# Optimization experiments

Hardware: AMD Instinct MI355X
Metric: run time of the kernel (lower is better)

Reference implementation:

```python
import jax, jax.numpy as jnp
import numpy as np

B_SZ, SEQ, H = 8, 1024, 2048
LN_EPS = 1e-6
CLIP = 1.0e6


def setup_inputs() -> dict:
    key = jax.random.key(0)
    ks = jax.random.split(key, 8)
    lecun = 1.0 / np.sqrt(H)
    return {
        "x": jax.random.normal(ks[0], (B_SZ, SEQ, H), dtype=jnp.float32),
        "context": jnp.zeros((B_SZ, H), dtype=jnp.float32),
        # learned params
        "A": -jax.random.uniform(ks[1], (H,), dtype=jnp.float32),  # diagonal decay (zeros-init in src; small negative for stable decay)
        "Bm": jax.random.normal(ks[2], (H, H), dtype=jnp.float32) * lecun,
        "Cm": jax.random.normal(ks[3], (H, H), dtype=jnp.float32) * lecun,
        "dt_kernel": jax.random.normal(ks[4], (H, 1), dtype=jnp.float32) * 0.02,
        "dt_bias": jnp.zeros((1,), dtype=jnp.float32),
        "gate_kernel": jax.random.normal(ks[5], (H, H), dtype=jnp.float32) * lecun,
        "gate_bias": jnp.zeros((H,), dtype=jnp.float32),
        "ln_scale": jnp.ones((H,), dtype=jnp.float32),
        "ln_bias": jnp.zeros((H,), dtype=jnp.float32),
    }


def _layernorm(x, scale, bias):
    mu = jnp.mean(x, axis=-1, keepdims=True)
    var = jnp.mean(jnp.square(x - mu), axis=-1, keepdims=True)
    return (x - mu) * jax.lax.rsqrt(var + LN_EPS) * scale + bias


def reference(x, context, A, Bm, Cm, dt_kernel, dt_bias, gate_kernel, gate_bias, ln_scale, ln_bias):
    xn = jnp.clip(_layernorm(x, ln_scale, ln_bias), -CLIP, CLIP)  # [B,S,H]
    xt = jnp.swapaxes(xn, 0, 1)  # time-major [S,B,H]

    def step(state, x_t):
        # x_t: [B,H]; delta: [B,1] from Dense(1)
        delta = jnp.exp(x_t @ dt_kernel + dt_bias)
        decay = jnp.exp(delta * A)                  # [B,H] via broadcast
        new_state = state * decay + x_t @ Bm        # [B,H]
        out = new_state @ Cm                        # [B,H]
        return new_state, out

    final_state, ys = jax.lax.scan(step, context, xt)
    outputs = jnp.swapaxes(ys, 0, 1)  # [B,S,H]
    gate = outputs @ gate_kernel + gate_bias
    outputs = outputs * jax.nn.sigmoid(gate)  # GLU
    # dropout deterministic (training=False) -> identity
    return outputs, final_state
```

## Files before the change

kernel.cpp:

```cpp
#include <hip/hip_runtime.h>
#include <hip/hip_bf16.h>

#define H_DIM 2048
#define B_SZ  8
#define SEQ   1024
#define M_DIM (B_SZ*SEQ)
#define KDIM  2048
#define NKT   (KDIM/64)
#define CCH   32
#define CLEN  (SEQ/CCH)

using f32x4 = __attribute__((ext_vector_type(4))) float;
using s16x8 = __attribute__((ext_vector_type(8))) short;

__device__ __forceinline__ float bf2f(unsigned short u) {
  unsigned int x = ((unsigned int)u) << 16;
  return __builtin_bit_cast(float, x);
}
__device__ __forceinline__ unsigned short f2bf(float f) {
  unsigned int x = __builtin_bit_cast(unsigned int, f);
  unsigned int r = (x + 0x7fffu + ((x >> 16) & 1u)) >> 16;
  return (unsigned short)r;
}

__device__ __forceinline__ void gl_lds16(const void* g, void* l) {
  __builtin_amdgcn_global_load_lds(
      (__attribute__((address_space(1))) void*)g,
      (__attribute__((address_space(3))) void*)l, 16, 0, 0);
}

__global__ __launch_bounds__(256) void transpose_kernel(
    const float* __restrict__ src, unsigned short* __restrict__ dst, int R, int C)
{
  __shared__ float t[32][33];
  int tx = threadIdx.x & 31, ty = threadIdx.x >> 5;
  int c0 = blockIdx.x << 5, r0 = blockIdx.y << 5;
#pragma unroll
  for (int i = 0; i < 32; i += 8)
    t[ty + i][tx] = src[(size_t)(r0 + ty + i) * C + (c0 + tx)];
  __syncthreads();
#pragma unroll
  for (int i = 0; i < 32; i += 8)
    dst[(size_t)(c0 + ty + i) * R + (r0 + tx)] = f2bf(t[tx][ty + i]);
}

__global__ __launch_bounds__(256) void ln_delta_kernel(
    const float* __restrict__ x, const float* __restrict__ lns,
    const float* __restrict__ lnb, const float* __restrict__ dtk,
    const float* __restrict__ dtb, unsigned short* __restrict__ xn,
    float* __restrict__ delta)
{
  const int row = blockIdx.x;
  const int tid = threadIdx.x;
  const float* xr = x + (size_t)row * H_DIM;
  float v[8];
  *(float4*)&v[0] = ((const float4*)xr)[tid * 2];
  *(float4*)&v[4] = ((const float4*)xr)[tid * 2 + 1];
  float s1 = 0.f, s2 = 0.f;
#pragma unroll
  for (int j = 0; j < 8; ++j) { s1 += v[j]; s2 += v[j] * v[j]; }
  __shared__ float red[8];
#pragma unroll
  for (int off = 32; off; off >>= 1) {
    s1 += __shfl_down(s1, off);
    s2 += __shfl_down(s2, off);
  }
  if ((tid & 63) == 0) { red[tid >> 6] = s1; red[4 + (tid >> 6)] = s2; }
  __syncthreads();
  float mean = (red[0] + red[1] + red[2] + red[3]) * (1.0f / H_DIM);
  float var  = (red[4] + red[5] + red[6] + red[7]) * (1.0f / H_DIM) - mean * mean;
  float rstd = rsqrtf(var + 1e-6f);

  float sc[8], bi[8], dk[8];
  *(float4*)&sc[0] = ((const float4*)lns)[tid * 2];
  *(float4*)&sc[4] = ((const float4*)lns)[tid * 2 + 1];
  *(float4*)&bi[0] = ((const float4*)lnb)[tid * 2];
  *(float4*)&bi[4] = ((const float4*)lnb)[tid * 2 + 1];
  *(float4*)&dk[0] = ((const float4*)dtk)[tid * 2];
  *(float4*)&dk[4] = ((const float4*)dtk)[tid * 2 + 1];

  float dot = 0.f;
  s16x8 o;
#pragma unroll
  for (int j = 0; j < 8; ++j) {
    float xv = (v[j] - mean) * rstd * sc[j] + bi[j];
    xv = fminf(fmaxf(xv, -1.0e6f), 1.0e6f);
    dot += xv * dk[j];
    o[j] = (short)f2bf(xv);
  }
  *(s16x8*)(xn + (size_t)row * H_DIM + tid * 8) = o;

  __syncthreads();
#pragma unroll
  for (int off = 32; off; off >>= 1) dot += __shfl_down(dot, off);
  if ((tid & 63) == 0) red[tid >> 6] = dot;
  __syncthreads();
  if (tid == 0)
    delta[row] = __expf(red[0] + red[1] + red[2] + red[3] + dtb[0]);
}

__global__ __launch_bounds__(256) void scan1_kernel(
    const unsigned short* __restrict__ U, const float* __restrict__ delta,
    const float* __restrict__ Adiag, float* __restrict__ Q, float* __restrict__ P)
{
  const int h = blockIdx.x * 1024 + threadIdx.x * 4;
  const int c = blockIdx.y, b = blockIdx.z;
  const float4 a = *(const float4*)(Adiag + h);
  const unsigned short* u = U + ((size_t)b * SEQ + c * CLEN) * H_DIM + h;
  const float* dl = delta + b * SEQ + c * CLEN;
  float4 st = {0.f, 0.f, 0.f, 0.f};
  float4 pr = {1.f, 1.f, 1.f, 1.f};
#pragma unroll 8
  for (int s = 0; s < CLEN; ++s) {
    const float d = dl[s];
    const ushort4 uv = *(const ushort4*)(u + (size_t)s * H_DIM);
    const float dx = __expf(d * a.x), dy = __expf(d * a.y);
    const float dz = __expf(d * a.z), dw = __expf(d * a.w);
    st.x = fmaf(st.x, dx, bf2f(uv.x)); st.y = fmaf(st.y, dy, bf2f(uv.y));
    st.z = fmaf(st.z, dz, bf2f(uv.z)); st.w = fmaf(st.w, dw, bf2f(uv.w));
    pr.x *= dx; pr.y *= dy; pr.z *= dz; pr.w *= dw;
  }
  const size_t idx = ((size_t)b * CCH + c) * H_DIM + h;
  *(float4*)(Q + idx) = st;
  *(float4*)(P + idx) = pr;
}

__global__ __launch_bounds__(256) void scan2_kernel(
    const float* __restrict__ Q, const float* __restrict__ P,
    const float* __restrict__ ctx, float* __restrict__ sIn,
    float* __restrict__ finalSt)
{
  const int h = blockIdx.x * 256 + threadIdx.x;
  const int b = blockIdx.y;
  float s = ctx[b * H_DIM + h];
#pragma unroll
  for (int c = 0; c < CCH; ++c) {
    const size_t idx = ((size_t)b * CCH + c) * H_DIM + h;
    sIn[idx] = s;
    s = fmaf(s, P[idx], Q[idx]);
  }
  finalSt[b * H_DIM + h] = s;
}

__global__ __launch_bounds__(256) void scan3_kernel(
    const unsigned short* __restrict__ U, const float* __restrict__ delta,
    const float* __restrict__ Adiag, const float* __restrict__ sIn,
    unsigned short* __restrict__ states)
{
  const int h = blockIdx.x * 1024 + threadIdx.x * 4;
  const int c = blockIdx.y, b = blockIdx.z;
  const float4 a = *(const float4*)(Adiag + h);
  const unsigned short* u = U + ((size_t)b * SEQ + c * CLEN) * H_DIM + h;
  unsigned short* so = states + ((size_t)b * SEQ + c * CLEN) * H_DIM + h;
  const float* dl = delta + b * SEQ + c * CLEN;
  float4 st = *(const float4*)(sIn + ((size_t)b * CCH + c) * H_DIM + h);
#pragma unroll 8
  for (int s = 0; s < CLEN; ++s) {
    const float d = dl[s];
    const ushort4 uv = *(const ushort4*)(u + (size_t)s * H_DIM);
    const float dx = __expf(d * a.x), dy = __expf(d * a.y);
    const float dz = __expf(d * a.z), dw = __expf(d * a.w);
    st.x = fmaf(st.x, dx, bf2f(uv.x)); st.y = fmaf(st.y, dy, bf2f(uv.y));
    st.z = fmaf(st.z, dz, bf2f(uv.z)); st.w = fmaf(st.w, dw, bf2f(uv.w));
    ushort4 ov = { f2bf(st.x), f2bf(st.y), f2bf(st.z), f2bf(st.w) };
    *(ushort4*)(so + (size_t)s * H_DIM) = ov;
  }
}


#define BARR()  __builtin_amdgcn_s_barrier();
#define VMC(N)  asm volatile("s_waitcnt vmcnt(" #N ")" ::: "memory");

#define RD_A(DST, PL, PHH, OFF) { _Pragma("unroll") for (int i_ = 0; i_ < 4; ++i_) { \
    DST[0][i_] = *(const s16x8*)((PL) + (OFF) + i_ * 4096); \
    DST[1][i_] = *(const s16x8*)((PHH) + (OFF) + i_ * 4096); } }
#define RD_B(DST, PL, PHH, OFF) { _Pragma("unroll") for (int j_ = 0; j_ < 2; ++j_) { \
    DST[0][j_] = *(const s16x8*)((PL) + (OFF) + j_ * 8192); \
    DST[1][j_] = *(const s16x8*)((PHH) + (OFF) + j_ * 8192); } }

#define QMM(IB, JB, AF, BF) { __builtin_amdgcn_s_setprio(1); \
  _Pragma("unroll") for (int i_ = 0; i_ < 4; ++i_) \
  _Pragma("unroll") for (int j_ = 0; j_ < 2; ++j_) { \
    acc[(IB)+i_][(JB)+j_] = __builtin_amdgcn_mfma_f32_16x16x32_bf16(AF[0][i_], BF[0][j_], acc[(IB)+i_][(JB)+j_], 0, 0, 0); \
    acc[(IB)+i_][(JB)+j_] = __builtin_amdgcn_mfma_f32_16x16x32_bf16(AF[1][i_], BF[1][j_], acc[(IB)+i_][(JB)+j_], 0, 0, 0); } \
  __builtin_amdgcn_s_setprio(0); }

#define STAGE_A(BUF, HH, TT) { const char* s_ = srcA + (HH) * 524288 + (TT) * 128; \
  char* d_ = ldsA + (BUF) * 32768 + (HH) * 16384 + tid16; \
  gl_lds16(s_, d_); gl_lds16(s_ + 262144, d_ + 8192); }
#define STAGE_B(BUF, HH, TT) { const char* s_ = srcB + (HH) * 524288 + (TT) * 128; \
  char* d_ = ldsB + (BUF) * 32768 + (HH) * 16384 + tid16; \
  gl_lds16(s_, d_); gl_lds16(s_ + 262144, d_ + 8192); }

template <int EPI>
__global__ __launch_bounds__(512, 2) void gemm8p(
    const char* __restrict__ Ab, const char* __restrict__ Bb,
    float* __restrict__ outF, unsigned short* __restrict__ outH,
    const unsigned short* __restrict__ Ybf, const float* __restrict__ gbias)
{
  extern __shared__ char lds[];
  char* ldsA = lds;
  char* ldsB = lds + 65536;

  const int tid  = threadIdx.x;
  const int lane = tid & 63, wid = tid >> 6;
  const int wr = wid >> 2, wc = wid & 3;
  const int fr = lane & 15, kq = lane >> 4;

  const int bid = blockIdx.x;
  const int xcd = bid & 7;
  const int li  = bid >> 3;
  const int bm  = (xcd >> 1) * 8 + (li & 7);
  const int bn  = (xcd & 1) * 4 + (li >> 3);

  const int grow = tid >> 3;
  const int gswz = ((tid & 7) ^ (grow & 7)) << 4;
  const char* srcA = Ab + ((size_t)(bm * 256 + grow)) * 4096 + gswz;
  const char* srcB = Bb + ((size_t)(bn * 256 + grow)) * 4096 + gswz;
  const int tid16 = tid << 4;

  const int sw0 = ((kq ^ (fr & 7)) << 4);
  const int sw1 = (((4 | kq) ^ (fr & 7)) << 4);
  const char* pa0b0 = ldsA + wr * 2048 + fr * 128 + sw0;
  const char* pa1b0 = ldsA + wr * 2048 + fr * 128 + sw1;
  const char* pa0b1 = pa0b0 + 32768;
  const char* pa1b1 = pa1b0 + 32768;
  const char* pb0b0 = ldsB + wc * 2048 + fr * 128 + sw0;
  const char* pb1b0 = ldsB + wc * 2048 + fr * 128 + sw1;
  const char* pb0b1 = pb0b0 + 32768;
  const char* pb1b1 = pb1b0 + 32768;

  f32x4 acc[8][4] = {};
  s16x8 a03[2][4], a47[2][4], b01a[2][2], b01b[2][2], b23[2][2];

  STAGE_A(0, 0, 0); STAGE_B(0, 0, 0); STAGE_B(0, 1, 0); STAGE_A(0, 1, 0);
  STAGE_A(1, 0, 1); STAGE_B(1, 0, 1); STAGE_B(1, 1, 1);
  VMC(6);
  BARR();
  RD_A(a03, pa0b0, pa1b0, 0);
  RD_B(b01a, pb0b0, pb1b0, 0);

  for (int t = 0; t < NKT / 2 - 1; ++t) {
    const int T0 = 2 * t;
    RD_B(b23, pb0b0, pb1b0, 16384);
    STAGE_A(1, 1, T0 + 1);
    QMM(0, 0, a03, b01a);
    VMC(6); BARR();
    RD_A(a47, pa0b0, pa1b0, 16384);
    STAGE_A(0, 0, T0 + 2);
    QMM(0, 2, a03, b23);
    VMC(6); BARR();
    RD_B(b01b, pb0b1, pb1b1, 0);
    STAGE_B(0, 0, T0 + 2);
    QMM(4, 0, a47, b01a);
    VMC(6); BARR();
    RD_A(a03, pa0b1, pa1b1, 0);
    STAGE_B(0, 1, T0 + 2);
    QMM(4, 2, a47, b23);
    VMC(6); BARR();
    RD_B(b23, pb0b1, pb1b1, 16384);
    STAGE_A(0, 1, T0 + 2);
    QMM(0, 0, a03, b01b);
    VMC(6); BARR();
    RD_A(a47, pa0b1, pa1b1, 16384);
    STAGE_A(1, 0, T0 + 3);
    QMM(0, 2, a03, b23);
    VMC(6); BARR();
    RD_B(b01a, pb0b0, pb1b0, 0);
    STAGE_B(1, 0, T0 + 3);
    QMM(4, 0, a47, b01b);
    VMC(6); BARR();
    RD_A(a03, pa0b0, pa1b0, 0);
    STAGE_B(1, 1, T0 + 3);
    QMM(4, 2, a47, b23);
    VMC(6); BARR();
  }

  RD_B(b23, pb0b0, pb1b0, 16384);
  STAGE_A(1, 1, 31);
  QMM(0, 0, a03, b01a);
  VMC(6); BARR();
  RD_A(a47, pa0b0, pa1b0, 16384);
  QMM(0, 2, a03, b23);
  VMC(0); BARR();
  RD_B(b01b, pb0b1, pb1b1, 0);
  QMM(4, 0, a47, b01a);
  RD_A(a03, pa0b1, pa1b1, 0);
  QMM(4, 2, a47, b23);
  RD_B(b23, pb0b1, pb1b1, 16384);
  QMM(0, 0, a03, b01b);
  RD_A(a47, pa0b1, pa1b1, 16384);
  QMM(0, 2, a03, b23);
  QMM(4, 0, a47, b01b);
  QMM(4, 2, a47, b23);

  __syncthreads();
  const int cr = (lane >> 4) << 2;
  const int cc = lane & 15;
  if constexpr (EPI == 1) {
#pragma unroll
    for (int i = 0; i < 8; ++i)
#pragma unroll
      for (int j = 0; j < 4; ++j)
#pragma unroll
        for (int r = 0; r < 4; ++r) {
          const int row = (2 * i + wr) * 16 + cr + r;
          const int col = (4 * j + wc) * 16 + cc;
          const int off = (row * 512 + col * 2) ^ ((row & 7) << 4);
          *(unsigned short*)(lds + off) = f2bf(acc[i][j][r]);
        }
    __syncthreads();
#pragma unroll
    for (int it = 0; it < 16; ++it) {
      const int L = it * 8192 + tid * 16;
      const int row = L >> 9, inrow = L & 511;
      const s16x8 v = *(const s16x8*)(lds + (L ^ ((row & 7) << 4)));
      *(s16x8*)(outH + ((size_t)(bm * 256 + row)) * H_DIM + bn * 256 + (inrow >> 1)) = v;
    }
  } else {
#pragma unroll
    for (int p = 0; p < 2; ++p) {
      if (p) __syncthreads();
#pragma unroll
      for (int i = 4 * p; i < 4 * p + 4; ++i)
#pragma unroll
        for (int j = 0; j < 4; ++j)
#pragma unroll
          for (int r = 0; r < 4; ++r) {
            const int lrow = (2 * i + wr) * 16 + cr + r - 128 * p;
            const int col = (4 * j + wc) * 16 + cc;
            const int off = (lrow * 1024 + col * 4) ^ ((lrow & 7) << 4);
            *(float*)(lds + off) = acc[i][j][r];
          }
      __syncthreads();
#pragma unroll
      for (int it = 0; it < 16; ++it) {
        const int L = it * 8192 + tid * 16;
        const int lrow = L >> 10, inrow = L & 1023;
        const f32x4 v = *(const f32x4*)(lds + (L ^ ((lrow & 7) << 4)));
        const size_t growg = (size_t)(bm * 256 + 128 * p + lrow);
        const int gcol = bn * 256 + (inrow >> 2);
        const float4 gb4 = *(const float4*)(gbias + gcol);
        const ushort4 y4 = *(const ushort4*)(Ybf + growg * H_DIM + gcol);
        float4 o;
        o.x = bf2f(y4.x) / (1.f + __expf(-(v[0] + gb4.x)));
        o.y = bf2f(y4.y) / (1.f + __expf(-(v[1] + gb4.y)));
        o.z = bf2f(y4.z) / (1.f + __expf(-(v[2] + gb4.z)));
        o.w = bf2f(y4.w) / (1.f + __expf(-(v[3] + gb4.w)));
        *(float4*)(outF + growg * H_DIM + gcol) = o;
      }
    }
  }
}

extern "C" void kernel_launch(void* const* d_in, const int* in_sizes, int n_in,
                              void* d_out, int out_size, void* d_ws, size_t ws_size,
                              hipStream_t stream) {
  (void)in_sizes; (void)n_in; (void)out_size; (void)ws_size;
  const float* x     = (const float*)d_in[0];
  const float* ctx   = (const float*)d_in[1];
  const float* Adiag = (const float*)d_in[2];
  const float* Bm    = (const float*)d_in[3];
  const float* Cm    = (const float*)d_in[4];
  const float* dtk   = (const float*)d_in[5];
  const float* dtb   = (const float*)d_in[6];
  const float* gk    = (const float*)d_in[7];
  const float* gb    = (const float*)d_in[8];
  const float* lns   = (const float*)d_in[9];
  const float* lnb   = (const float*)d_in[10];
  float* outF = (float*)d_out;

  char* ws = (char*)d_ws;
  unsigned short* xnY    = (unsigned short*)ws; ws += (size_t)M_DIM * H_DIM * 2;
  unsigned short* U      = (unsigned short*)ws; ws += (size_t)M_DIM * H_DIM * 2;
  unsigned short* states = (unsigned short*)ws; ws += (size_t)M_DIM * H_DIM * 2;
  unsigned short* T1     = (unsigned short*)ws; ws += (size_t)H_DIM * H_DIM * 2;
  unsigned short* T2     = (unsigned short*)ws; ws += (size_t)H_DIM * H_DIM * 2;
  unsigned short* T3     = (unsigned short*)ws; ws += (size_t)H_DIM * H_DIM * 2;
  float* delta           = (float*)ws;          ws += (size_t)M_DIM * 4;
  float* Qbuf            = (float*)ws;          ws += (size_t)B_SZ * CCH * H_DIM * 4;
  float* Pbuf            = (float*)ws;          ws += (size_t)B_SZ * CCH * H_DIM * 4;
  float* sInBuf          = (float*)ws;          ws += (size_t)B_SZ * CCH * H_DIM * 4;

  hipFuncSetAttribute((const void*)&gemm8p<1>,
                      hipFuncAttributeMaxDynamicSharedMemorySize, 131072);
  hipFuncSetAttribute((const void*)&gemm8p<2>,
                      hipFuncAttributeMaxDynamicSharedMemorySize, 131072);

  dim3 tb(256);
  transpose_kernel<<<dim3(64, 64), tb, 0, stream>>>(Bm, T1, H_DIM, H_DIM);
  transpose_kernel<<<dim3(64, 64), tb, 0, stream>>>(Cm, T2, H_DIM, H_DIM);
  transpose_kernel<<<dim3(64, 64), tb, 0, stream>>>(gk, T3, H_DIM, H_DIM);
  ln_delta_kernel<<<M_DIM, tb, 0, stream>>>(x, lns, lnb, dtk, dtb, xnY, delta);
  gemm8p<1><<<256, 512, 131072, stream>>>(
      (const char*)xnY, (const char*)T1, nullptr, U, nullptr, nullptr);
  scan1_kernel<<<dim3(H_DIM / 1024, CCH, B_SZ), tb, 0, stream>>>(
      U, delta, Adiag, Qbuf, Pbuf);
  scan2_kernel<<<dim3(H_DIM / 256, B_SZ), tb, 0, stream>>>(
      Qbuf, Pbuf, ctx, sInBuf, outF + (size_t)M_DIM * H_DIM);
  scan3_kernel<<<dim3(H_DIM / 1024, CCH, B_SZ), tb, 0, stream>>>(
      U, delta, Adiag, sInBuf, states);
  gemm8p<1><<<256, 512, 131072, stream>>>(
      (const char*)states, (const char*)T2, nullptr, xnY, nullptr, nullptr);
  gemm8p<2><<<256, 512, 131072, stream>>>(
      (const char*)xnY, (const char*)T3, outF, nullptr, xnY, gb);
}
```

Measured before the change: 259.7 us.

## Switch GEMM inner loop from 16x16x32 to 32x32x16 bf16 MFMA tiles

Rewrites the GEMM's fragment loads, MFMA calls and epilogue writeback to use 32x32x16 bf16 MFMA instructions instead of 16x16x32. Each wave now holds a 4x2 grid of 32x32 accumulators. Fragments are read per 32-row slab with a new swizzled K-offset table. Larger MFMA tiles cut the number of LDS fragment reads per FLOP and the instruction issue overhead. The risk is a different register footprint and possible LDS bank conflicts from the new access pattern.

```diff
diff --git a/kernel.cpp b/kernel.cpp
--- a/kernel.cpp
+++ b/kernel.cpp
@@ -10,8 +10,9 @@
 #define CCH   32
 #define CLEN  (SEQ/CCH)
 
-using f32x4 = __attribute__((ext_vector_type(4))) float;
-using s16x8 = __attribute__((ext_vector_type(8))) short;
+using f32x4  = __attribute__((ext_vector_type(4))) float;
+using f32x16 = __attribute__((ext_vector_type(16))) float;
+using s16x8  = __attribute__((ext_vector_type(8))) short;
 
 __device__ __forceinline__ float bf2f(unsigned short u) {
   unsigned int x = ((unsigned int)u) << 16;
@@ -171,18 +172,16 @@
 #define BARR()  __builtin_amdgcn_s_barrier();
 #define VMC(N)  asm volatile("s_waitcnt vmcnt(" #N ")" ::: "memory");
 
-#define RD_A(DST, PL, PHH, OFF) { _Pragma("unroll") for (int i_ = 0; i_ < 4; ++i_) { \
-    DST[0][i_] = *(const s16x8*)((PL) + (OFF) + i_ * 4096); \
-    DST[1][i_] = *(const s16x8*)((PHH) + (OFF) + i_ * 4096); } }
-#define RD_B(DST, PL, PHH, OFF) { _Pragma("unroll") for (int j_ = 0; j_ < 2; ++j_) { \
-    DST[0][j_] = *(const s16x8*)((PL) + (OFF) + j_ * 8192); \
-    DST[1][j_] = *(const s16x8*)((PHH) + (OFF) + j_ * 8192); } }
-
-#define QMM(IB, JB, AF, BF) { __builtin_amdgcn_s_setprio(1); \
-  _Pragma("unroll") for (int i_ = 0; i_ < 4; ++i_) \
-  _Pragma("unroll") for (int j_ = 0; j_ < 2; ++j_) { \
-    acc[(IB)+i_][(JB)+j_] = __builtin_amdgcn_mfma_f32_16x16x32_bf16(AF[0][i_], BF[0][j_], acc[(IB)+i_][(JB)+j_], 0, 0, 0); \
-    acc[(IB)+i_][(JB)+j_] = __builtin_amdgcn_mfma_f32_16x16x32_bf16(AF[1][i_], BF[1][j_], acc[(IB)+i_][(JB)+j_], 0, 0, 0); } \
+#define RD_AM(DST, BUF, MQ) { _Pragma("unroll") for (int m_ = 0; m_ < 2; ++m_) \
+  _Pragma("unroll") for (int s_ = 0; s_ < 4; ++s_) \
+    DST[m_][s_] = *(const s16x8*)(paA + (BUF) * 32768 + (MQ) * 16384 + m_ * 8192 + soff[s_]); }
+#define RD_BN(DST, BUF, N) { _Pragma("unroll") for (int s_ = 0; s_ < 4; ++s_) \
+    DST[s_] = *(const s16x8*)(pbB + (BUF) * 32768 + (N) * 16384 + soff[s_]); }
+
+#define QMM(AF, BF, MI, NI) { __builtin_amdgcn_s_setprio(1); \
+  _Pragma("unroll") for (int m_ = 0; m_ < 2; ++m_) \
+  _Pragma("unroll") for (int s_ = 0; s_ < 4; ++s_) \
+    acc[(MI)+m_][NI] = __builtin_amdgcn_mfma_f32_32x32x16_bf16(AF[m_][s_], BF[s_], acc[(MI)+m_][NI], 0, 0, 0); \
   __builtin_amdgcn_s_setprio(0); }
 
 #define STAGE_A(BUF, HH, TT) { const char* s_ = srcA + (HH) * 524288 + (TT) * 128; \
@@ -205,7 +204,7 @@
   const int tid  = threadIdx.x;
   const int lane = tid & 63, wid = tid >> 6;
   const int wr = wid >> 2, wc = wid & 3;
-  const int fr = lane & 15, kq = lane >> 4;
+  const int ln31 = lane & 31, l5 = lane >> 5;
 
   const int bid = blockIdx.x;
   const int xcd = bid & 7;
@@ -219,95 +218,90 @@
   const char* srcB = Bb + ((size_t)(bn * 256 + grow)) * 4096 + gswz;
   const int tid16 = tid << 4;
 
-  const int sw0 = ((kq ^ (fr & 7)) << 4);
-  const int sw1 = (((4 | kq) ^ (fr & 7)) << 4);
-  const char* pa0b0 = ldsA + wr * 2048 + fr * 128 + sw0;
-  const char* pa1b0 = ldsA + wr * 2048 + fr * 128 + sw1;
-  const char* pa0b1 = pa0b0 + 32768;
-  const char* pa1b1 = pa1b0 + 32768;
-  const char* pb0b0 = ldsB + wc * 2048 + fr * 128 + sw0;
-  const char* pb1b0 = ldsB + wc * 2048 + fr * 128 + sw1;
-  const char* pb0b1 = pb0b0 + 32768;
-  const char* pb1b1 = pb1b0 + 32768;
-
-  f32x4 acc[8][4] = {};
-  s16x8 a03[2][4], a47[2][4], b01a[2][2], b01b[2][2], b23[2][2];
+  const char* paA = ldsA + wr * 4096 + ln31 * 128;
+  const char* pbB = ldsB + (wc * 32 + ln31) * 128;
+  int soff[4];
+#pragma unroll
+  for (int s = 0; s < 4; ++s)
+    soff[s] = ((2 * s + l5) ^ (ln31 & 7)) << 4;
+
+  f32x16 acc[4][2] = {};
+  s16x8 aA[2][4], aB[2][4], bA[4], bB[4], bA2[4];
 
   STAGE_A(0, 0, 0); STAGE_B(0, 0, 0); STAGE_B(0, 1, 0); STAGE_A(0, 1, 0);
   STAGE_A(1, 0, 1); STAGE_B(1, 0, 1); STAGE_B(1, 1, 1);
   VMC(6);
   BARR();
-  RD_A(a03, pa0b0, pa1b0, 0);
-  RD_B(b01a, pb0b0, pb1b0, 0);
+  RD_AM(aA, 0, 0);
+  RD_BN(bA, 0, 0);
 
   for (int t = 0; t < NKT / 2 - 1; ++t) {
     const int T0 = 2 * t;
-    RD_B(b23, pb0b0, pb1b0, 16384);
+    RD_BN(bB, 0, 1);
     STAGE_A(1, 1, T0 + 1);
-    QMM(0, 0, a03, b01a);
-    VMC(6); BARR();
-    RD_A(a47, pa0b0, pa1b0, 16384);
+    QMM(aA, bA, 0, 0);
+    VMC(6); BARR();
+    RD_AM(aB, 0, 1);
     STAGE_A(0, 0, T0 + 2);
-    QMM(0, 2, a03, b23);
-    VMC(6); BARR();
-    RD_B(b01b, pb0b1, pb1b1, 0);
+    QMM(aA, bB, 0, 1);
+    VMC(6); BARR();
+    RD_BN(bA2, 1, 0);
     STAGE_B(0, 0, T0 + 2);
-    QMM(4, 0, a47, b01a);
-    VMC(6); BARR();
-    RD_A(a03, pa0b1, pa1b1, 0);
+    QMM(aB, bA, 2, 0);
+    VMC(6); BARR();
+    RD_AM(aA, 1, 0);
     STAGE_B(0, 1, T0 + 2);
-    QMM(4, 2, a47, b23);
-    VMC(6); BARR();
-    RD_B(b23, pb0b1, pb1b1, 16384);
+    QMM(aB, bB, 2, 1);
+    VMC(6); BARR();
+    RD_BN(bB, 1, 1);
     STAGE_A(0, 1, T0 + 2);
-    QMM(0, 0, a03, b01b);
-    VMC(6); BARR();
-    RD_A(a47, pa0b1, pa1b1, 16384);
+    QMM(aA, bA2, 0, 0);
+    VMC(6); BARR();
+    RD_AM(aB, 1, 1);
     STAGE_A(1, 0, T0 + 3);
-    QMM(0, 2, a03, b23);
-    VMC(6); BARR();
-    RD_B(b01a, pb0b0, pb1b0, 0);
+    QMM(aA, bB, 0, 1);
+    VMC(6); BARR();
+    RD_BN(bA, 0, 0);
     STAGE_B(1, 0, T0 + 3);
-    QMM(4, 0, a47, b01b);
-    VMC(6); BARR();
-    RD_A(a03, pa0b0, pa1b0, 0);
+    QMM(aB, bA2, 2, 0);
+    VMC(6); BARR();
+    RD_AM(aA, 0, 0);
     STAGE_B(1, 1, T0 + 3);
-    QMM(4, 2, a47, b23);
-    VMC(6); BARR();
-  }
-
-  RD_B(b23, pb0b0, pb1b0, 16384);
+    QMM(aB, bB, 2, 1);
+    VMC(6); BARR();
+  }
+
+  RD_BN(bB, 0, 1);
   STAGE_A(1, 1, 31);
-  QMM(0, 0, a03, b01a);
+  QMM(aA, bA, 0, 0);
   VMC(6); BARR();
-  RD_A(a47, pa0b0, pa1b0, 16384);
-  QMM(0, 2, a03, b23);
+  RD_AM(aB, 0, 1);
+  QMM(aA, bB, 0, 1);
   VMC(0); BARR();
-  RD_B(b01b, pb0b1, pb1b1, 0);
-  QMM(4, 0, a47, b01a);
-  RD_A(a03, pa0b1, pa1b1, 0);
-  QMM(4, 2, a47, b23);
-  RD_B(b23, pb0b1, pb1b1, 16384);
-  QMM(0, 0, a03, b01b);
-  RD_A(a47, pa0b1, pa1b1, 16384);
-  QMM(0, 2, a03, b23);
-  QMM(4, 0, a47, b01b);
-  QMM(4, 2, a47, b23);
+  RD_BN(bA2, 1, 0);
+  QMM(aB, bA, 2, 0);
+  RD_AM(aA, 1, 0);
+  QMM(aB, bB, 2, 1);
+  RD_BN(bB, 1, 1);
+  QMM(aA, bA2, 0, 0);
+  RD_AM(aB, 1, 1);
+  QMM(aA, bB, 0, 1);
+  QMM(aB, bA2, 2, 0);
+  QMM(aB, bB, 2, 1);
 
   __syncthreads();
-  const int cr = (lane >> 4) << 2;
-  const int cc = lane & 15;
   if constexpr (EPI == 1) {
 #pragma unroll
-    for (int i = 0; i < 8; ++i)
-#pragma unroll
-      for (int j = 0; j < 4; ++j)
-#pragma unroll
-        for (int r = 0; r < 4; ++r) {
-          const int row = (2 * i + wr) * 16 + cr + r;
-          const int col = (4 * j + wc) * 16 + cc;
+    for (int mi = 0; mi < 4; ++mi)
+#pragma unroll
+      for (int n = 0; n < 2; ++n)
+#pragma unroll
+        for (int reg = 0; reg < 16; ++reg) {
+          const int rowin = (reg & 3) + 8 * (reg >> 2) + 4 * l5;
+          const int row = (4 * (mi >> 1) + 2 * (mi & 1) + wr) * 32 + rowin;
+          const int col = n * 128 + wc * 32 + ln31;
           const int off = (row * 512 + col * 2) ^ ((row & 7) << 4);
-          *(unsigned short*)(lds + off) = f2bf(acc[i][j][r]);
+          *(unsigned short*)(lds + off) = f2bf(acc[mi][n][reg]);
         }
     __syncthreads();
 #pragma unroll
@@ -322,15 +316,16 @@
     for (int p = 0; p < 2; ++p) {
       if (p) __syncthreads();
 #pragma unroll
-      for (int i = 4 * p; i < 4 * p + 4; ++i)
-#pragma unroll
-        for (int j = 0; j < 4; ++j)
-#pragma unroll
-          for (int r = 0; r < 4; ++r) {
-            const int lrow = (2 * i + wr) * 16 + cr + r - 128 * p;
-            const int col = (4 * j + wc) * 16 + cc;
+      for (int mi = 2 * p; mi < 2 * p + 2; ++mi)
+#pragma unroll
+        for (int n = 0; n < 2; ++n)
+#pragma unroll
+          for (int reg = 0; reg < 16; ++reg) {
+            const int rowin = (reg & 3) + 8 * (reg >> 2) + 4 * l5;
+            const int lrow = (2 * (mi & 1) + wr) * 32 + rowin;
+            const int col = n * 128 + wc * 32 + ln31;
             const int off = (lrow * 1024 + col * 4) ^ ((lrow & 7) << 4);
-            *(float*)(lds + off) = acc[i][j][r];
+            *(float*)(lds + off) = acc[mi][n][reg];
           }
       __syncthreads();
 #pragma unroll
```

Result: slower. 278.0 us (+7.0%).
